# Optimization experiments

Hardware: AMD Instinct MI355X
Metric: run time of the kernel (lower is better)

Reference implementation:

```python
import jax, jax.numpy as jnp
import numpy as np
from jax import lax

B, T, D = 1, 2048, 2048
H, KVH, HD = 16, 4, 128
BETA = 0.9
ROPE_BASE = 10000.0


def _causal_prefix_ema(x, beta):
    # x: (B, T, D); m_t = beta * m_{t-1} + (1 - beta) * x_t, m_{-1} = 0
    def step(m, xt):
        m = beta * m + (1.0 - beta) * xt
        return m, m
    _, ys = lax.scan(step, jnp.zeros_like(x[:, 0]), jnp.swapaxes(x, 0, 1))
    return jnp.swapaxes(ys, 0, 1)


def _rotate_half(x):
    x1, x2 = jnp.split(x, 2, axis=-1)
    return jnp.concatenate([-x2, x1], axis=-1)


def _rope_cos_sin(t, hd, dtype):
    inv_freq = 1.0 / (ROPE_BASE ** (jnp.arange(0, hd, 2, dtype=jnp.float32) / hd))
    freqs = jnp.arange(t, dtype=jnp.float32)[:, None] * inv_freq[None, :]  # (T, HD/2)
    emb = jnp.concatenate([freqs, freqs], axis=-1)  # (T, HD)
    return jnp.cos(emb).astype(dtype)[None, None], jnp.sin(emb).astype(dtype)[None, None]


def setup_inputs() -> dict:
    key = jax.random.key(0)
    ks = jax.random.split(key, 8)
    std = 0.02
    return {
        "hidden_states": jax.random.normal(ks[0], (B, T, D), jnp.float32),
        "Wq": jax.random.normal(ks[1], (D, H * HD), jnp.float32) * std,
        "Wk": jax.random.normal(ks[2], (D, KVH * HD), jnp.float32) * std,
        "Wv": jax.random.normal(ks[3], (D, KVH * HD), jnp.float32) * std,
        "Wo": jax.random.normal(ks[4], (H * HD, D), jnp.float32) * std,
        "Wr1": jax.random.normal(ks[5], (D, D // 2), jnp.float32) * std,
        "br1": jnp.zeros((D // 2,), jnp.float32),
        "Wr2": jax.random.normal(ks[6], (D // 2, 2), jnp.float32) * std,
        "br2": jnp.zeros((2,), jnp.float32),
    }


def reference(hidden_states, Wq, Wk, Wv, Wo, Wr1, br1, Wr2, br2):
    b, t, d = hidden_states.shape
    q = hidden_states @ Wq  # (B, T, H*HD)

    # multi-level memories: l1 = raw, l2 = causal prefix EMA
    l2 = _causal_prefix_ema(hidden_states, BETA)

    # router MLP on q + softmax over levels
    h = jax.nn.silu(q @ Wr1 + br1)
    lam = jax.nn.softmax(h @ Wr2 + br2, axis=-1)  # (B, T, 2)
    fused = lam[..., 0:1] * hidden_states + lam[..., 1:2] * l2

    # shape to heads
    q_s = q.reshape(b, t, H, HD).transpose(0, 2, 1, 3)                 # (B, H, T, HD)
    k_s = (fused @ Wk).reshape(b, t, KVH, HD).transpose(0, 2, 1, 3)    # (B, KVH, T, HD)
    v_s = (fused @ Wv).reshape(b, t, KVH, HD).transpose(0, 2, 1, 3)

    # RoPE
    cos, sin = _rope_cos_sin(t, HD, q_s.dtype)
    q_s = q_s * cos + _rotate_half(q_s) * sin
    k_s = k_s * cos + _rotate_half(k_s) * sin

    # repeat kv for GQA
    n_rep = H // KVH
    k_s = jnp.repeat(k_s, n_rep, axis=1)
    v_s = jnp.repeat(v_s, n_rep, axis=1)

    # causal SDPA
    scale = 1.0 / jnp.sqrt(jnp.asarray(HD, q_s.dtype))
    scores = jnp.einsum("bhqd,bhkd->bhqk", q_s, k_s) * scale
    causal = jnp.tril(jnp.ones((t, t), dtype=bool))
    scores = jnp.where(causal[None, None], scores, jnp.finfo(scores.dtype).min)
    attn = jax.nn.softmax(scores, axis=-1)
    out = jnp.einsum("bhqk,bhkd->bhqd", attn, v_s)  # (B, H, T, HD)

    out = out.transpose(0, 2, 1, 3).reshape(b, t, H * HD)
    return out @ Wo
```

## Files before the change

kernel.cpp:

```cpp
#include <hip/hip_runtime.h>
#include <hip/hip_bf16.h>

#define T_SEQ 2048
#define D_MODEL 2048
#define NH 16
#define NKVH 4
#define HD 128

typedef __attribute__((ext_vector_type(8))) short bf16x8;
typedef __attribute__((ext_vector_type(4))) float f32x4;

static __device__ __forceinline__ short f32_to_bf16(float f) {
    unsigned u = __float_as_uint(f);
    u += 0x7fffu + ((u >> 16) & 1u);
    return (short)(u >> 16);
}
static __device__ __forceinline__ float bf16_to_f32(short s) {
    return __uint_as_float(((unsigned)(unsigned short)s) << 16);
}
static __device__ __forceinline__ void gl_to_lds16(const void* g, void* l) {
    __builtin_amdgcn_global_load_lds(
        (const __attribute__((address_space(1))) unsigned int*)g,
        (__attribute__((address_space(3))) unsigned int*)l, 16, 0, 0);
}

template<int BN>
__global__ __launch_bounds__(256, 2) void gemm_bt_kernel(
    const short* __restrict__ A, const short* __restrict__ Bt,
    float* __restrict__ Cf, short* __restrict__ Cb,
    int M, int N, int K, const float* __restrict__ bias, int act)
{
    constexpr int NI = BN / 64;
    constexpr int BCH = BN / 32;
    __shared__ short Alds[2][64 * 64];
    __shared__ short Blds[2][BN * 64];

    const int tid = threadIdx.x;
    const int wave = tid >> 6, lane = tid & 63;
    const int l16 = lane & 15, quad = lane >> 4;
    const int wn = wave * (BN / 4);
    const int m0 = blockIdx.y * 64, n0 = blockIdx.x * BN;
    const int niter = K >> 6;

    f32x4 acc[4][NI] = {};

    #pragma unroll
    for (int p = 0; p < 2; ++p) {
        int li = p * 256 + tid;
        int row = li >> 3, sc = li & 7;
        gl_to_lds16(A + (size_t)(m0 + row) * K + ((sc ^ (row & 7)) * 8),
                    &Alds[0][(size_t)(p * 256 + wave * 64) * 8]);
    }
    #pragma unroll
    for (int p = 0; p < BCH; ++p) {
        int li = p * 256 + tid;
        int row = li >> 3, sc = li & 7;
        gl_to_lds16(Bt + (size_t)(n0 + row) * K + ((sc ^ (row & 7)) * 8),
                    &Blds[0][(size_t)(p * 256 + wave * 64) * 8]);
    }

    for (int t = 0; t < niter; ++t) {
        asm volatile("s_waitcnt vmcnt(0)\n\ts_barrier" ::: "memory");

        if (t + 1 < niter) {
            int k1 = (t + 1) << 6;
            int nb = (t + 1) & 1;
            #pragma unroll
            for (int p = 0; p < 2; ++p) {
                int li = p * 256 + tid;
                int row = li >> 3, sc = li & 7;
                gl_to_lds16(A + (size_t)(m0 + row) * K + k1 + ((sc ^ (row & 7)) * 8),
                            &Alds[nb][(size_t)(p * 256 + wave * 64) * 8]);
            }
            #pragma unroll
            for (int p = 0; p < BCH; ++p) {
                int li = p * 256 + tid;
                int row = li >> 3, sc = li & 7;
                gl_to_lds16(Bt + (size_t)(n0 + row) * K + k1 + ((sc ^ (row & 7)) * 8),
                            &Blds[nb][(size_t)(p * 256 + wave * 64) * 8]);
            }
        }

        const short* Ab = Alds[t & 1];
        const short* Bb = Blds[t & 1];
        #pragma unroll
        for (int kk = 0; kk < 2; ++kk) {
            bf16x8 a[4], b[NI];
            #pragma unroll
            for (int i = 0; i < 4; ++i)
                a[i] = *(const bf16x8*)
                    &Ab[(size_t)(i * 16 + l16) * 64 + (((kk * 4 + quad) ^ (l16 & 7)) * 8)];
            #pragma unroll
            for (int i = 0; i < NI; ++i)
                b[i] = *(const bf16x8*)
                    &Bb[(size_t)(wn + i * 16 + l16) * 64 + (((kk * 4 + quad) ^ (l16 & 7)) * 8)];
            #pragma unroll
            for (int mi = 0; mi < 4; ++mi)
                #pragma unroll
                for (int ni = 0; ni < NI; ++ni)
                    acc[mi][ni] = __builtin_amdgcn_mfma_f32_16x16x32_bf16(
                        a[mi], b[ni], acc[mi][ni], 0, 0, 0);
        }
    }

    #pragma unroll
    for (int mi = 0; mi < 4; ++mi) {
        #pragma unroll
        for (int ni = 0; ni < NI; ++ni) {
            int col = n0 + wn + ni * 16 + l16;
            float bv = bias ? bias[col] : 0.0f;
            #pragma unroll
            for (int r = 0; r < 4; ++r) {
                int row = m0 + mi * 16 + quad * 4 + r;
                float x = acc[mi][ni][r] + bv;
                if (act) x = x / (1.0f + __expf(-x));
                size_t o = (size_t)row * N + col;
                if (Cf) Cf[o] = x;
                if (Cb) Cb[o] = f32_to_bf16(x);
            }
        }
    }
}

__global__ __launch_bounds__(256) void transpose_all_kernel(
    const float* __restrict__ Wq, const float* __restrict__ Wk,
    const float* __restrict__ Wv, const float* __restrict__ Wr1,
    const float* __restrict__ Wo, short* __restrict__ Wq_t,
    short* __restrict__ Wkv_t, short* __restrict__ Wr1_t,
    short* __restrict__ Wo_t)
{
    __shared__ float tile[32][33];
    int bx = blockIdx.x;
    const float* src; short* dst; int ld, cb;
    if (bx < 64)       { src = Wq;  dst = Wq_t;  ld = 2048; cb = bx; }
    else if (bx < 80)  { src = Wk;  dst = Wkv_t; ld = 512;  cb = bx - 64; }
    else if (bx < 96)  { src = Wv;  dst = Wkv_t + (size_t)512 * 2048; ld = 512; cb = bx - 80; }
    else if (bx < 128) { src = Wr1; dst = Wr1_t; ld = 1024; cb = bx - 96; }
    else               { src = Wo;  dst = Wo_t;  ld = 2048; cb = bx - 128; }
    int c0 = cb * 32, r0 = blockIdx.y * 32;
    int t = threadIdx.x;
    int r = t >> 3, c4 = (t & 7) * 4;
    float4 v = *(const float4*)&src[(size_t)(r0 + r) * ld + c0 + c4];
    tile[r][c4 + 0] = v.x; tile[r][c4 + 1] = v.y;
    tile[r][c4 + 2] = v.z; tile[r][c4 + 3] = v.w;
    __syncthreads();
    short o[4];
    #pragma unroll
    for (int j = 0; j < 4; ++j) o[j] = f32_to_bf16(tile[c4 + j][r]);
    *(uint2*)&dst[(size_t)(c0 + r) * 2048 + r0 + c4] = *(const uint2*)o;
}

__global__ __launch_bounds__(256) void transpose_bf_kernel(
    const short* __restrict__ src, int ld, short* __restrict__ dst, int ldd)
{
    __shared__ float tile[32][33];
    int r0 = blockIdx.y * 32, c0 = blockIdx.x * 32;
    int x = threadIdx.x & 31, y = threadIdx.x >> 5;
    #pragma unroll
    for (int i = 0; i < 4; ++i)
        tile[y + i * 8][x] = bf16_to_f32(src[(size_t)(r0 + y + i * 8) * ld + c0 + x]);
    __syncthreads();
    #pragma unroll
    for (int i = 0; i < 4; ++i)
        dst[(size_t)(c0 + y + i * 8) * ldd + r0 + x] = f32_to_bf16(tile[x][y + i * 8]);
}

__global__ __launch_bounds__(256) void ema_kernel(const float* __restrict__ hs,
                                                  float* __restrict__ l2,
                                                  short* __restrict__ hs_b)
{
    int d = blockIdx.y * 256 + threadIdx.x;
    int t0 = blockIdx.x * 128;
    int ts = t0 - 192; if (ts < 0) ts = 0;
    float m = 0.0f;
    for (int tb = ts; tb < t0; tb += 16) {
        float buf[16];
        #pragma unroll
        for (int j = 0; j < 16; ++j) buf[j] = hs[(size_t)(tb + j) * D_MODEL + d];
        #pragma unroll
        for (int j = 0; j < 16; ++j) m = 0.9f * m + 0.1f * buf[j];
    }
    for (int tb = t0; tb < t0 + 128; tb += 16) {
        float buf[16];
        #pragma unroll
        for (int j = 0; j < 16; ++j) buf[j] = hs[(size_t)(tb + j) * D_MODEL + d];
        #pragma unroll
        for (int j = 0; j < 16; ++j) hs_b[(size_t)(tb + j) * D_MODEL + d] = f32_to_bf16(buf[j]);
        #pragma unroll
        for (int j = 0; j < 16; ++j) { m = 0.9f * m + 0.1f * buf[j]; buf[j] = m; }
        #pragma unroll
        for (int j = 0; j < 16; ++j) l2[(size_t)(tb + j) * D_MODEL + d] = buf[j];
    }
}

__global__ __launch_bounds__(64) void lam_kernel(
    const short* __restrict__ h, const float* __restrict__ Wr2,
    const float* __restrict__ br2, float* __restrict__ lam)
{
    int t = blockIdx.x;
    int lane = threadIdx.x;
    float z0 = 0.0f, z1 = 0.0f;
    for (int i = lane; i < 1024; i += 64) {
        float hv = bf16_to_f32(h[(size_t)t * 1024 + i]);
        z0 += hv * Wr2[i * 2 + 0];
        z1 += hv * Wr2[i * 2 + 1];
    }
    #pragma unroll
    for (int off = 1; off < 64; off <<= 1) {
        z0 += __shfl_xor(z0, off);
        z1 += __shfl_xor(z1, off);
    }
    if (lane == 0) {
        z0 += br2[0]; z1 += br2[1];
        float mx = fmaxf(z0, z1);
        float e0 = expf(z0 - mx), e1 = expf(z1 - mx);
        float inv = 1.0f / (e0 + e1);
        lam[t * 2 + 0] = e0 * inv;
        lam[t * 2 + 1] = e1 * inv;
    }
}

__global__ void fuse_kernel(const float* __restrict__ hs, const float* __restrict__ l2,
                            const float* __restrict__ lam, short* __restrict__ fused)
{
    int idx = blockIdx.x * blockDim.x + threadIdx.x;
    int t = idx >> 9;
    float a0 = lam[t * 2 + 0], a1 = lam[t * 2 + 1];
    float4 a = ((const float4*)hs)[idx];
    float4 b = ((const float4*)l2)[idx];
    short o[4] = {f32_to_bf16(a0 * a.x + a1 * b.x), f32_to_bf16(a0 * a.y + a1 * b.y),
                  f32_to_bf16(a0 * a.z + a1 * b.z), f32_to_bf16(a0 * a.w + a1 * b.w)};
    *(uint2*)(fused + (size_t)idx * 4) = *(const uint2*)o;
}

__global__ void rope_q_kernel(const short* __restrict__ q, short* __restrict__ qr)
{
    int idx = blockIdx.x * blockDim.x + threadIdx.x;
    int d = idx & 63;
    int h = (idx >> 6) & 15;
    int t = idx >> 10;
    float fr = (float)t * __expf(-(float)d * 0.14391156831212787f);
    float s, c;
    sincosf(fr, &s, &c);
    const float sc = 0.08838834764831845f;
    const short* src = q + (size_t)t * D_MODEL + h * HD;
    float x1 = bf16_to_f32(src[d]) * sc, x2 = bf16_to_f32(src[d + 64]) * sc;
    short* dst = qr + ((size_t)h * T_SEQ + t) * HD;
    dst[d]      = f32_to_bf16(x1 * c - x2 * s);
    dst[d + 64] = f32_to_bf16(x2 * c + x1 * s);
}

__global__ void rope_k_kernel(const short* __restrict__ kv, short* __restrict__ kr)
{
    int idx = blockIdx.x * blockDim.x + threadIdx.x;
    int d = idx & 63;
    int kh = (idx >> 6) & 3;
    int t = idx >> 8;
    float fr = (float)t * __expf(-(float)d * 0.14391156831212787f);
    float s, c;
    sincosf(fr, &s, &c);
    const short* src = kv + (size_t)t * 1024 + kh * HD;
    float x1 = bf16_to_f32(src[d]), x2 = bf16_to_f32(src[d + 64]);
    short* dst = kr + ((size_t)kh * T_SEQ + t) * HD;
    dst[d]      = f32_to_bf16(x1 * c - x2 * s);
    dst[d + 64] = f32_to_bf16(x2 * c + x1 * s);
}

__global__ __launch_bounds__(256, 1) void attn_kernel(
    const short* __restrict__ Qr, const short* __restrict__ Kr,
    const short* __restrict__ Vt, short* __restrict__ Out)
{
    const int pi = blockIdx.x;
    const int h = blockIdx.y;
    const int kvh = h >> 2;
    const int tid = threadIdx.x;
    const int wave = tid >> 6, lane = tid & 63;
    const int l16 = lane & 15, quad = lane >> 4;

    __shared__ short Klds[2][128 * 128];
    __shared__ short Vlds[2][128 * 128];
    __shared__ short Plds[4][16][136];

    const short* kbase = Kr + (size_t)kvh * T_SEQ * HD;
    const short* vbase = Vt + (size_t)kvh * HD * T_SEQ;

    for (int ph = 0; ph < 2; ++ph) {
        const int qt = ph ? (31 - pi) : pi;
        const int qbase = qt * 64 + wave * 16;
        const int n = (qt * 64 + 191) >> 7;

        bf16x8 qf[4];
        {
            const short* qrow = Qr + ((size_t)h * T_SEQ + qbase + l16) * HD;
            #pragma unroll
            for (int kc = 0; kc < 4; ++kc)
                qf[kc] = *(const bf16x8*)&qrow[kc * 32 + quad * 8];
        }
        f32x4 o[8] = {};
        float lsum[4] = {0.0f, 0.0f, 0.0f, 0.0f};

        __syncthreads();

        {
            const short* ks = kbase;
            #pragma unroll
            for (int p = 0; p < 8; ++p) {
                int li = p * 256 + tid;
                int row = li >> 4, gs = (li & 15) ^ (row & 15);
                gl_to_lds16(ks + (size_t)row * HD + gs * 8,
                            &Klds[0][(size_t)(p * 256 + wave * 64) * 8]);
            }
            #pragma unroll
            for (int p = 0; p < 8; ++p) {
                int li = p * 256 + tid;
                int row = li >> 4, gs = (li & 15) ^ (row & 15);
                gl_to_lds16(vbase + (size_t)row * T_SEQ + gs * 8,
                            &Vlds[0][(size_t)(p * 256 + wave * 64) * 8]);
            }
        }

        for (int t = 0; t < n; ++t) {
            asm volatile("s_waitcnt vmcnt(0)\n\ts_barrier" ::: "memory");

            if (t + 1 < n) {
                int kv1 = (t + 1) << 7;
                int nb = (t + 1) & 1;
                const short* ks = kbase + (size_t)kv1 * HD;
                #pragma unroll
                for (int p = 0; p < 8; ++p) {
                    int li = p * 256 + tid;
                    int row = li >> 4, gs = (li & 15) ^ (row & 15);
                    gl_to_lds16(ks + (size_t)row * HD + gs * 8,
                                &Klds[nb][(size_t)(p * 256 + wave * 64) * 8]);
                }
                #pragma unroll
                for (int p = 0; p < 8; ++p) {
                    int li = p * 256 + tid;
                    int row = li >> 4, gs = (li & 15) ^ (row & 15);
                    gl_to_lds16(vbase + (size_t)row * T_SEQ + kv1 + gs * 8,
                                &Vlds[nb][(size_t)(p * 256 + wave * 64) * 8]);
                }
            }

            const short* Kb = Klds[t & 1];
            const short* Vb = Vlds[t & 1];

            f32x4 s[8];
            #pragma unroll
            for (int ni = 0; ni < 8; ++ni) s[ni] = (f32x4){0, 0, 0, 0};
            #pragma unroll
            for (int ni = 0; ni < 8; ++ni)
                #pragma unroll
                for (int kc = 0; kc < 4; ++kc) {
                    bf16x8 b = *(const bf16x8*)
                        &Kb[(size_t)(ni * 16 + l16) * 128 + (((kc * 4 + quad) ^ l16) * 8)];
                    s[ni] = __builtin_amdgcn_mfma_f32_16x16x32_bf16(qf[kc], b, s[ni], 0, 0, 0);
                }

            if (t == n - 1) {
                int kvg0 = t << 7;
                #pragma unroll
                for (int ni = 0; ni < 8; ++ni) {
                    int kvg = kvg0 + ni * 16 + l16;
                    #pragma unroll
                    for (int r = 0; r < 4; ++r) {
                        int qg = qbase + quad * 4 + r;
                        float p = (kvg <= qg) ? __expf(s[ni][r]) : 0.0f;
                        lsum[r] += p;
                        Plds[wave][quad * 4 + r][ni * 16 + l16] = f32_to_bf16(p);
                    }
                }
            } else {
                #pragma unroll
                for (int ni = 0; ni < 8; ++ni)
                    #pragma unroll
                    for (int r = 0; r < 4; ++r) {
                        float p = __expf(s[ni][r]);
                        lsum[r] += p;
                        Plds[wave][quad * 4 + r][ni * 16 + l16] = f32_to_bf16(p);
                    }
            }
            asm volatile("s_waitcnt lgkmcnt(0)" ::: "memory");

            #pragma unroll
            for (int d8 = 0; d8 < 8; ++d8)
                #pragma unroll
                for (int r = 0; r < 4; ++r) o[d8][r] *= 1.0f;
            #pragma unroll
            for (int kc = 0; kc < 4; ++kc) {
                bf16x8 pa = *(const bf16x8*)&Plds[wave][l16][kc * 32 + quad * 8];
                #pragma unroll
                for (int d8 = 0; d8 < 8; ++d8) {
                    bf16x8 b = *(const bf16x8*)
                        &Vb[(size_t)(d8 * 16 + l16) * 128 + (((kc * 4 + quad) ^ l16) * 8)];
                    o[d8] = __builtin_amdgcn_mfma_f32_16x16x32_bf16(pa, b, o[d8], 0, 0, 0);
                }
            }
        }

        #pragma unroll
        for (int r = 0; r < 4; ++r) {
            #pragma unroll
            for (int off = 1; off < 16; off <<= 1)
                lsum[r] += __shfl_xor(lsum[r], off);
            lsum[r] = 1.0f / lsum[r];
        }
        #pragma unroll
        for (int d8 = 0; d8 < 8; ++d8)
            #pragma unroll
            for (int r = 0; r < 4; ++r) {
                int row = qbase + quad * 4 + r;
                Out[(size_t)row * D_MODEL + h * HD + d8 * 16 + l16] =
                    f32_to_bf16(o[d8][r] * lsum[r]);
            }
    }
}

extern "C" void kernel_launch(void* const* d_in, const int* in_sizes, int n_in,
                              void* d_out, int out_size, void* d_ws, size_t ws_size,
                              hipStream_t stream)
{
    const float* hs  = (const float*)d_in[0];
    const float* Wq  = (const float*)d_in[1];
    const float* Wk  = (const float*)d_in[2];
    const float* Wv  = (const float*)d_in[3];
    const float* Wo  = (const float*)d_in[4];
    const float* Wr1 = (const float*)d_in[5];
    const float* br1 = (const float*)d_in[6];
    const float* Wr2 = (const float*)d_in[7];
    const float* br2 = (const float*)d_in[8];
    float* out = (float*)d_out;

    char* w = (char*)d_ws;
    const size_t MB = 1u << 20;
    float* l2_f     = (float*)(w + 0 * MB);
    short* hs_bf    = (short*)(w + 16 * MB);
    short* Wq_t     = (short*)(w + 24 * MB);
    short* Wkv_t    = (short*)(w + 32 * MB);
    short* Wr1_t    = (short*)(w + 36 * MB);
    short* Wo_t     = (short*)(w + 40 * MB);
    short* q_bf     = (short*)(w + 48 * MB);
    short* h_bf     = (short*)(w + 56 * MB);
    short* fused_bf = (short*)(w + 60 * MB);
    short* kv_bf    = (short*)(w + 68 * MB);
    short* qr       = (short*)(w + 72 * MB);
    short* kr       = (short*)(w + 80 * MB);
    short* vr       = (short*)(w + 82 * MB);
    float* lam_f    = (float*)(w + 84 * MB);
    short* attn_bf  = hs_bf;

    transpose_all_kernel<<<dim3(192, 64), 256, 0, stream>>>(
        Wq, Wk, Wv, Wr1, Wo, Wq_t, Wkv_t, Wr1_t, Wo_t);

    ema_kernel<<<dim3(T_SEQ / 128, D_MODEL / 256), 256, 0, stream>>>(hs, l2_f, hs_bf);

    gemm_bt_kernel<128><<<dim3(16, 32), 256, 0, stream>>>(
        hs_bf, Wq_t, nullptr, q_bf, 2048, 2048, 2048, nullptr, 0);

    gemm_bt_kernel<64><<<dim3(16, 32), 256, 0, stream>>>(
        q_bf, Wr1_t, nullptr, h_bf, 2048, 1024, 2048, br1, 1);

    lam_kernel<<<T_SEQ, 64, 0, stream>>>(h_bf, Wr2, br2, lam_f);

    fuse_kernel<<<(T_SEQ * D_MODEL / 4) / 256, 256, 0, stream>>>(hs, l2_f, lam_f, fused_bf);

    gemm_bt_kernel<64><<<dim3(16, 32), 256, 0, stream>>>(
        fused_bf, Wkv_t, nullptr, kv_bf, 2048, 1024, 2048, nullptr, 0);

    rope_q_kernel<<<(T_SEQ * NH * 64) / 256, 256, 0, stream>>>(q_bf, qr);
    rope_k_kernel<<<(T_SEQ * NKVH * 64) / 256, 256, 0, stream>>>(kv_bf, kr);
    transpose_bf_kernel<<<dim3(16, 64), 256, 0, stream>>>(kv_bf + 512, 1024, vr, 2048);

    attn_kernel<<<dim3(16, NH), 256, 0, stream>>>(qr, kr, vr, attn_bf);

    gemm_bt_kernel<128><<<dim3(16, 32), 256, 0, stream>>>(
        attn_bf, Wo_t, out, nullptr, 2048, 2048, 2048, nullptr, 0);
}
```

Measured before the change: 318.0 us.

## Use 8-wave attention blocks over 128-row query tiles with swizzled P and setprio

The attention kernel changes from 4-wave blocks that each process two paired 64-row query tiles (balanced front and back) to 8-wave blocks that each process one 128-row query tile. Each staged K/V tile is now shared by twice as many waves, and the extra waves give more latency hiding. It also XOR-swizzles the P scratch buffer in LDS to avoid bank conflicts and raises wave priority around the MFMA sections. The cost is that the front/back pairing is gone, so causal work per block now ranges from 1 to 16 KV tiles and the grid becomes load-imbalanced.

```diff
diff --git a/kernel.cpp b/kernel.cpp
--- a/kernel.cpp
+++ b/kernel.cpp
@@ -266,11 +266,11 @@
     dst[d + 64] = f32_to_bf16(x2 * c + x1 * s);
 }
 
-__global__ __launch_bounds__(256, 1) void attn_kernel(
+__global__ __launch_bounds__(512, 2) void attn_kernel(
     const short* __restrict__ Qr, const short* __restrict__ Kr,
     const short* __restrict__ Vt, short* __restrict__ Out)
 {
-    const int pi = blockIdx.x;
+    const int qt = blockIdx.x;
     const int h = blockIdx.y;
     const int kvh = h >> 2;
     const int tid = threadIdx.x;
@@ -279,141 +279,140 @@
 
     __shared__ short Klds[2][128 * 128];
     __shared__ short Vlds[2][128 * 128];
-    __shared__ short Plds[4][16][136];
+    __shared__ short Plds[8][16][128];
 
     const short* kbase = Kr + (size_t)kvh * T_SEQ * HD;
     const short* vbase = Vt + (size_t)kvh * HD * T_SEQ;
 
-    for (int ph = 0; ph < 2; ++ph) {
-        const int qt = ph ? (31 - pi) : pi;
-        const int qbase = qt * 64 + wave * 16;
-        const int n = (qt * 64 + 191) >> 7;
-
-        bf16x8 qf[4];
-        {
-            const short* qrow = Qr + ((size_t)h * T_SEQ + qbase + l16) * HD;
-            #pragma unroll
-            for (int kc = 0; kc < 4; ++kc)
-                qf[kc] = *(const bf16x8*)&qrow[kc * 32 + quad * 8];
-        }
-        f32x4 o[8] = {};
-        float lsum[4] = {0.0f, 0.0f, 0.0f, 0.0f};
-
-        __syncthreads();
-
-        {
-            const short* ks = kbase;
-            #pragma unroll
-            for (int p = 0; p < 8; ++p) {
-                int li = p * 256 + tid;
+    const int qbase = qt * 128 + wave * 16;
+    const int n = qt + 1;
+
+    bf16x8 qf[4];
+    {
+        const short* qrow = Qr + ((size_t)h * T_SEQ + qbase + l16) * HD;
+        #pragma unroll
+        for (int kc = 0; kc < 4; ++kc)
+            qf[kc] = *(const bf16x8*)&qrow[kc * 32 + quad * 8];
+    }
+    f32x4 o[8] = {};
+    float lsum[4] = {0.0f, 0.0f, 0.0f, 0.0f};
+
+    {
+        #pragma unroll
+        for (int p = 0; p < 4; ++p) {
+            int li = p * 512 + tid;
+            int row = li >> 4, gs = (li & 15) ^ (row & 15);
+            gl_to_lds16(kbase + (size_t)row * HD + gs * 8,
+                        &Klds[0][(size_t)(p * 512 + wave * 64) * 8]);
+        }
+        #pragma unroll
+        for (int p = 0; p < 4; ++p) {
+            int li = p * 512 + tid;
+            int row = li >> 4, gs = (li & 15) ^ (row & 15);
+            gl_to_lds16(vbase + (size_t)row * T_SEQ + gs * 8,
+                        &Vlds[0][(size_t)(p * 512 + wave * 64) * 8]);
+        }
+    }
+
+    for (int t = 0; t < n; ++t) {
+        asm volatile("s_waitcnt vmcnt(0)\n\ts_barrier" ::: "memory");
+
+        if (t + 1 < n) {
+            int kv1 = (t + 1) << 7;
+            int nb = (t + 1) & 1;
+            const short* ks = kbase + (size_t)kv1 * HD;
+            #pragma unroll
+            for (int p = 0; p < 4; ++p) {
+                int li = p * 512 + tid;
                 int row = li >> 4, gs = (li & 15) ^ (row & 15);
                 gl_to_lds16(ks + (size_t)row * HD + gs * 8,
-                            &Klds[0][(size_t)(p * 256 + wave * 64) * 8]);
-            }
-            #pragma unroll
-            for (int p = 0; p < 8; ++p) {
-                int li = p * 256 + tid;
+                            &Klds[nb][(size_t)(p * 512 + wave * 64) * 8]);
+            }
+            #pragma unroll
+            for (int p = 0; p < 4; ++p) {
+                int li = p * 512 + tid;
                 int row = li >> 4, gs = (li & 15) ^ (row & 15);
-                gl_to_lds16(vbase + (size_t)row * T_SEQ + gs * 8,
-                            &Vlds[0][(size_t)(p * 256 + wave * 64) * 8]);
-            }
-        }
-
-        for (int t = 0; t < n; ++t) {
-            asm volatile("s_waitcnt vmcnt(0)\n\ts_barrier" ::: "memory");
-
-            if (t + 1 < n) {
-                int kv1 = (t + 1) << 7;
-                int nb = (t + 1) & 1;
-                const short* ks = kbase + (size_t)kv1 * HD;
+                gl_to_lds16(vbase + (size_t)row * T_SEQ + kv1 + gs * 8,
+                            &Vlds[nb][(size_t)(p * 512 + wave * 64) * 8]);
+            }
+        }
+
+        const short* Kb = Klds[t & 1];
+        const short* Vb = Vlds[t & 1];
+
+        f32x4 s[8];
+        #pragma unroll
+        for (int ni = 0; ni < 8; ++ni) s[ni] = (f32x4){0, 0, 0, 0};
+        __builtin_amdgcn_s_setprio(1);
+        #pragma unroll
+        for (int ni = 0; ni < 8; ++ni)
+            #pragma unroll
+            for (int kc = 0; kc < 4; ++kc) {
+                bf16x8 b = *(const bf16x8*)
+                    &Kb[(size_t)(ni * 16 + l16) * 128 + (((kc * 4 + quad) ^ l16) * 8)];
+                s[ni] = __builtin_amdgcn_mfma_f32_16x16x32_bf16(qf[kc], b, s[ni], 0, 0, 0);
+            }
+        __builtin_amdgcn_s_setprio(0);
+
+        if (t == n - 1) {
+            int kvg0 = t << 7;
+            #pragma unroll
+            for (int ni = 0; ni < 8; ++ni) {
+                int kvg = kvg0 + ni * 16 + l16;
                 #pragma unroll
-                for (int p = 0; p < 8; ++p) {
-                    int li = p * 256 + tid;
-                    int row = li >> 4, gs = (li & 15) ^ (row & 15);
-                    gl_to_lds16(ks + (size_t)row * HD + gs * 8,
-                                &Klds[nb][(size_t)(p * 256 + wave * 64) * 8]);
+                for (int r = 0; r < 4; ++r) {
+                    int qg = qbase + quad * 4 + r;
+                    float p = (kvg <= qg) ? __expf(s[ni][r]) : 0.0f;
+                    lsum[r] += p;
+                    int prow = quad * 4 + r, pcol = ni * 16 + l16;
+                    Plds[wave][prow][(((pcol >> 3) ^ prow) * 8) + (pcol & 7)] =
+                        f32_to_bf16(p);
                 }
-                #pragma unroll
-                for (int p = 0; p < 8; ++p) {
-                    int li = p * 256 + tid;
-                    int row = li >> 4, gs = (li & 15) ^ (row & 15);
-                    gl_to_lds16(vbase + (size_t)row * T_SEQ + kv1 + gs * 8,
-                                &Vlds[nb][(size_t)(p * 256 + wave * 64) * 8]);
-                }
-            }
-
-            const short* Kb = Klds[t & 1];
-            const short* Vb = Vlds[t & 1];
-
-            f32x4 s[8];
-            #pragma unroll
-            for (int ni = 0; ni < 8; ++ni) s[ni] = (f32x4){0, 0, 0, 0};
+            }
+        } else {
             #pragma unroll
             for (int ni = 0; ni < 8; ++ni)
                 #pragma unroll
-                for (int kc = 0; kc < 4; ++kc) {
-                    bf16x8 b = *(const bf16x8*)
-                        &Kb[(size_t)(ni * 16 + l16) * 128 + (((kc * 4 + quad) ^ l16) * 8)];
-                    s[ni] = __builtin_amdgcn_mfma_f32_16x16x32_bf16(qf[kc], b, s[ni], 0, 0, 0);
+                for (int r = 0; r < 4; ++r) {
+                    float p = __expf(s[ni][r]);
+                    lsum[r] += p;
+                    int prow = quad * 4 + r, pcol = ni * 16 + l16;
+                    Plds[wave][prow][(((pcol >> 3) ^ prow) * 8) + (pcol & 7)] =
+                        f32_to_bf16(p);
                 }
-
-            if (t == n - 1) {
-                int kvg0 = t << 7;
-                #pragma unroll
-                for (int ni = 0; ni < 8; ++ni) {
-                    int kvg = kvg0 + ni * 16 + l16;
-                    #pragma unroll
-                    for (int r = 0; r < 4; ++r) {
-                        int qg = qbase + quad * 4 + r;
-                        float p = (kvg <= qg) ? __expf(s[ni][r]) : 0.0f;
-                        lsum[r] += p;
-                        Plds[wave][quad * 4 + r][ni * 16 + l16] = f32_to_bf16(p);
-                    }
-                }
-            } else {
-                #pragma unroll
-                for (int ni = 0; ni < 8; ++ni)
-                    #pragma unroll
-                    for (int r = 0; r < 4; ++r) {
-                        float p = __expf(s[ni][r]);
-                        lsum[r] += p;
-                        Plds[wave][quad * 4 + r][ni * 16 + l16] = f32_to_bf16(p);
-                    }
-            }
-            asm volatile("s_waitcnt lgkmcnt(0)" ::: "memory");
-
-            #pragma unroll
-            for (int d8 = 0; d8 < 8; ++d8)
-                #pragma unroll
-                for (int r = 0; r < 4; ++r) o[d8][r] *= 1.0f;
-            #pragma unroll
-            for (int kc = 0; kc < 4; ++kc) {
-                bf16x8 pa = *(const bf16x8*)&Plds[wave][l16][kc * 32 + quad * 8];
-                #pragma unroll
-                for (int d8 = 0; d8 < 8; ++d8) {
-                    bf16x8 b = *(const bf16x8*)
-                        &Vb[(size_t)(d8 * 16 + l16) * 128 + (((kc * 4 + quad) ^ l16) * 8)];
-                    o[d8] = __builtin_amdgcn_mfma_f32_16x16x32_bf16(pa, b, o[d8], 0, 0, 0);
-                }
-            }
-        }
-
+        }
+        asm volatile("s_waitcnt lgkmcnt(0)" ::: "memory");
+
+        __builtin_amdgcn_s_setprio(1);
+        #pragma unroll
+        for (int kc = 0; kc < 4; ++kc) {
+            bf16x8 pa = *(const bf16x8*)
+                &Plds[wave][l16][(((kc * 4 + quad) ^ l16) * 8)];
+            #pragma unroll
+            for (int d8 = 0; d8 < 8; ++d8) {
+                bf16x8 b = *(const bf16x8*)
+                    &Vb[(size_t)(d8 * 16 + l16) * 128 + (((kc * 4 + quad) ^ l16) * 8)];
+                o[d8] = __builtin_amdgcn_mfma_f32_16x16x32_bf16(pa, b, o[d8], 0, 0, 0);
+            }
+        }
+        __builtin_amdgcn_s_setprio(0);
+    }
+
+    #pragma unroll
+    for (int r = 0; r < 4; ++r) {
+        #pragma unroll
+        for (int off = 1; off < 16; off <<= 1)
+            lsum[r] += __shfl_xor(lsum[r], off);
+        lsum[r] = 1.0f / lsum[r];
+    }
+    #pragma unroll
+    for (int d8 = 0; d8 < 8; ++d8)
         #pragma unroll
         for (int r = 0; r < 4; ++r) {
-            #pragma unroll
-            for (int off = 1; off < 16; off <<= 1)
-                lsum[r] += __shfl_xor(lsum[r], off);
-            lsum[r] = 1.0f / lsum[r];
-        }
-        #pragma unroll
-        for (int d8 = 0; d8 < 8; ++d8)
-            #pragma unroll
-            for (int r = 0; r < 4; ++r) {
-                int row = qbase + quad * 4 + r;
-                Out[(size_t)row * D_MODEL + h * HD + d8 * 16 + l16] =
-                    f32_to_bf16(o[d8][r] * lsum[r]);
-            }
-    }
+            int row = qbase + quad * 4 + r;
+            Out[(size_t)row * D_MODEL + h * HD + d8 * 16 + l16] =
+                f32_to_bf16(o[d8][r] * lsum[r]);
+        }
 }
 
 extern "C" void kernel_launch(void* const* d_in, const int* in_sizes, int n_in,
@@ -471,7 +470,7 @@
     rope_k_kernel<<<(T_SEQ * NKVH * 64) / 256, 256, 0, stream>>>(kv_bf, kr);
     transpose_bf_kernel<<<dim3(16, 64), 256, 0, stream>>>(kv_bf + 512, 1024, vr, 2048);
 
-    attn_kernel<<<dim3(16, NH), 256, 0, stream>>>(qr, kr, vr, attn_bf);
+    attn_kernel<<<dim3(16, NH), 512, 0, stream>>>(qr, kr, vr, attn_bf);
 
     gemm_bt_kernel<128><<<dim3(16, 32), 256, 0, stream>>>(
         attn_bf, Wo_t, out, nullptr, 2048, 2048, 2048, nullptr, 0);
```

New measurement: 323.7 us. About the same (+1.8%).

## Widen attention query tile to 128 rows per block with swizzled P buffer

Applied to the files above, without the earlier changes.

Each attention block now handles one 128-row query tile (32 rows per wave, two MFMA M-tiles) instead of two 64-row tiles paired for causal load balance. Every K/V tile loaded into LDS therefore feeds twice as much MFMA work, and the causal mask applies only on the final diagonal tile. The grid is reordered to heads-by-query-tile, the P staging buffer gets an XOR swizzle to avoid bank conflicts, and s_setprio is raised around the MFMA loops. The trade-offs are more registers per wave and uneven per-block work, since blocks run from 1 to 16 KV iterations, with no more paired balancing.

```diff
diff --git a/kernel.cpp b/kernel.cpp
--- a/kernel.cpp
+++ b/kernel.cpp
@@ -270,8 +270,8 @@
     const short* __restrict__ Qr, const short* __restrict__ Kr,
     const short* __restrict__ Vt, short* __restrict__ Out)
 {
-    const int pi = blockIdx.x;
-    const int h = blockIdx.y;
+    const int h = blockIdx.x;
+    const int qt = blockIdx.y;
     const int kvh = h >> 2;
     const int tid = threadIdx.x;
     const int wave = tid >> 6, lane = tid & 63;
@@ -279,141 +279,155 @@
 
     __shared__ short Klds[2][128 * 128];
     __shared__ short Vlds[2][128 * 128];
-    __shared__ short Plds[4][16][136];
+    __shared__ short Plds[4][32][128];
 
     const short* kbase = Kr + (size_t)kvh * T_SEQ * HD;
     const short* vbase = Vt + (size_t)kvh * HD * T_SEQ;
 
-    for (int ph = 0; ph < 2; ++ph) {
-        const int qt = ph ? (31 - pi) : pi;
-        const int qbase = qt * 64 + wave * 16;
-        const int n = (qt * 64 + 191) >> 7;
-
-        bf16x8 qf[4];
-        {
-            const short* qrow = Qr + ((size_t)h * T_SEQ + qbase + l16) * HD;
-            #pragma unroll
-            for (int kc = 0; kc < 4; ++kc)
-                qf[kc] = *(const bf16x8*)&qrow[kc * 32 + quad * 8];
-        }
-        f32x4 o[8] = {};
-        float lsum[4] = {0.0f, 0.0f, 0.0f, 0.0f};
-
-        __syncthreads();
-
-        {
-            const short* ks = kbase;
+    const int qbase = qt * 128 + wave * 32;
+    const int n = qt + 1;
+
+    bf16x8 qf[2][4];
+    #pragma unroll
+    for (int m = 0; m < 2; ++m) {
+        const short* qrow = Qr + ((size_t)h * T_SEQ + qbase + m * 16 + l16) * HD;
+        #pragma unroll
+        for (int kc = 0; kc < 4; ++kc)
+            qf[m][kc] = *(const bf16x8*)&qrow[kc * 32 + quad * 8];
+    }
+    f32x4 o[2][8] = {};
+    float lsum[2][4] = {};
+
+    {
+        #pragma unroll
+        for (int p = 0; p < 8; ++p) {
+            int li = p * 256 + tid;
+            int row = li >> 4, gs = (li & 15) ^ (row & 15);
+            gl_to_lds16(kbase + (size_t)row * HD + gs * 8,
+                        &Klds[0][(size_t)(p * 256 + wave * 64) * 8]);
+        }
+        #pragma unroll
+        for (int p = 0; p < 8; ++p) {
+            int li = p * 256 + tid;
+            int row = li >> 4, gs = (li & 15) ^ (row & 15);
+            gl_to_lds16(vbase + (size_t)row * T_SEQ + gs * 8,
+                        &Vlds[0][(size_t)(p * 256 + wave * 64) * 8]);
+        }
+    }
+
+    for (int t = 0; t < n; ++t) {
+        asm volatile("s_waitcnt vmcnt(0)\n\ts_barrier" ::: "memory");
+
+        if (t + 1 < n) {
+            int kv1 = (t + 1) << 7;
+            int nb = (t + 1) & 1;
+            const short* ks = kbase + (size_t)kv1 * HD;
             #pragma unroll
             for (int p = 0; p < 8; ++p) {
                 int li = p * 256 + tid;
                 int row = li >> 4, gs = (li & 15) ^ (row & 15);
                 gl_to_lds16(ks + (size_t)row * HD + gs * 8,
-                            &Klds[0][(size_t)(p * 256 + wave * 64) * 8]);
+                            &Klds[nb][(size_t)(p * 256 + wave * 64) * 8]);
             }
             #pragma unroll
             for (int p = 0; p < 8; ++p) {
                 int li = p * 256 + tid;
                 int row = li >> 4, gs = (li & 15) ^ (row & 15);
-                gl_to_lds16(vbase + (size_t)row * T_SEQ + gs * 8,
-                            &Vlds[0][(size_t)(p * 256 + wave * 64) * 8]);
-            }
-        }
-
-        for (int t = 0; t < n; ++t) {
-            asm volatile("s_waitcnt vmcnt(0)\n\ts_barrier" ::: "memory");
-
-            if (t + 1 < n) {
-                int kv1 = (t + 1) << 7;
-                int nb = (t + 1) & 1;
-                const short* ks = kbase + (size_t)kv1 * HD;
-                #pragma unroll
-                for (int p = 0; p < 8; ++p) {
-                    int li = p * 256 + tid;
-                    int row = li >> 4, gs = (li & 15) ^ (row & 15);
-                    gl_to_lds16(ks + (size_t)row * HD + gs * 8,
-                                &Klds[nb][(size_t)(p * 256 + wave * 64) * 8]);
-                }
-                #pragma unroll
-                for (int p = 0; p < 8; ++p) {
-                    int li = p * 256 + tid;
-                    int row = li >> 4, gs = (li & 15) ^ (row & 15);
-                    gl_to_lds16(vbase + (size_t)row * T_SEQ + kv1 + gs * 8,
-                                &Vlds[nb][(size_t)(p * 256 + wave * 64) * 8]);
-                }
-            }
-
-            const short* Kb = Klds[t & 1];
-            const short* Vb = Vlds[t & 1];
-
-            f32x4 s[8];
-            #pragma unroll
-            for (int ni = 0; ni < 8; ++ni) s[ni] = (f32x4){0, 0, 0, 0};
-            #pragma unroll
-            for (int ni = 0; ni < 8; ++ni)
-                #pragma unroll
-                for (int kc = 0; kc < 4; ++kc) {
-                    bf16x8 b = *(const bf16x8*)
-                        &Kb[(size_t)(ni * 16 + l16) * 128 + (((kc * 4 + quad) ^ l16) * 8)];
-                    s[ni] = __builtin_amdgcn_mfma_f32_16x16x32_bf16(qf[kc], b, s[ni], 0, 0, 0);
-                }
-
-            if (t == n - 1) {
-                int kvg0 = t << 7;
+                gl_to_lds16(vbase + (size_t)row * T_SEQ + kv1 + gs * 8,
+                            &Vlds[nb][(size_t)(p * 256 + wave * 64) * 8]);
+            }
+        }
+
+        const short* Kb = Klds[t & 1];
+        const short* Vb = Vlds[t & 1];
+
+        f32x4 s[2][8];
+        #pragma unroll
+        for (int m = 0; m < 2; ++m)
+            #pragma unroll
+            for (int ni = 0; ni < 8; ++ni) s[m][ni] = (f32x4){0, 0, 0, 0};
+        __builtin_amdgcn_s_setprio(1);
+        #pragma unroll
+        for (int ni = 0; ni < 8; ++ni)
+            #pragma unroll
+            for (int kc = 0; kc < 4; ++kc) {
+                bf16x8 b = *(const bf16x8*)
+                    &Kb[(size_t)(ni * 16 + l16) * 128 + (((kc * 4 + quad) ^ l16) * 8)];
+                s[0][ni] = __builtin_amdgcn_mfma_f32_16x16x32_bf16(qf[0][kc], b, s[0][ni], 0, 0, 0);
+                s[1][ni] = __builtin_amdgcn_mfma_f32_16x16x32_bf16(qf[1][kc], b, s[1][ni], 0, 0, 0);
+            }
+        __builtin_amdgcn_s_setprio(0);
+
+        if (t == n - 1) {
+            int kvg0 = t << 7;
+            #pragma unroll
+            for (int m = 0; m < 2; ++m)
                 #pragma unroll
                 for (int ni = 0; ni < 8; ++ni) {
                     int kvg = kvg0 + ni * 16 + l16;
                     #pragma unroll
                     for (int r = 0; r < 4; ++r) {
-                        int qg = qbase + quad * 4 + r;
-                        float p = (kvg <= qg) ? __expf(s[ni][r]) : 0.0f;
-                        lsum[r] += p;
-                        Plds[wave][quad * 4 + r][ni * 16 + l16] = f32_to_bf16(p);
+                        int qg = qbase + m * 16 + quad * 4 + r;
+                        float p = (kvg <= qg) ? __expf(s[m][ni][r]) : 0.0f;
+                        lsum[m][r] += p;
+                        int prow = quad * 4 + r, pcol = ni * 16 + l16;
+                        Plds[wave][m * 16 + prow][(((pcol >> 3) ^ prow) * 8) + (pcol & 7)] =
+                            f32_to_bf16(p);
                     }
                 }
-            } else {
+        } else {
+            #pragma unroll
+            for (int m = 0; m < 2; ++m)
                 #pragma unroll
                 for (int ni = 0; ni < 8; ++ni)
                     #pragma unroll
                     for (int r = 0; r < 4; ++r) {
-                        float p = __expf(s[ni][r]);
-                        lsum[r] += p;
-                        Plds[wave][quad * 4 + r][ni * 16 + l16] = f32_to_bf16(p);
+                        float p = __expf(s[m][ni][r]);
+                        lsum[m][r] += p;
+                        int prow = quad * 4 + r, pcol = ni * 16 + l16;
+                        Plds[wave][m * 16 + prow][(((pcol >> 3) ^ prow) * 8) + (pcol & 7)] =
+                            f32_to_bf16(p);
                     }
-            }
-            asm volatile("s_waitcnt lgkmcnt(0)" ::: "memory");
-
-            #pragma unroll
-            for (int d8 = 0; d8 < 8; ++d8)
-                #pragma unroll
-                for (int r = 0; r < 4; ++r) o[d8][r] *= 1.0f;
-            #pragma unroll
-            for (int kc = 0; kc < 4; ++kc) {
-                bf16x8 pa = *(const bf16x8*)&Plds[wave][l16][kc * 32 + quad * 8];
-                #pragma unroll
-                for (int d8 = 0; d8 < 8; ++d8) {
-                    bf16x8 b = *(const bf16x8*)
-                        &Vb[(size_t)(d8 * 16 + l16) * 128 + (((kc * 4 + quad) ^ l16) * 8)];
-                    o[d8] = __builtin_amdgcn_mfma_f32_16x16x32_bf16(pa, b, o[d8], 0, 0, 0);
-                }
-            }
-        }
-
+        }
+        asm volatile("s_waitcnt lgkmcnt(0)" ::: "memory");
+
+        __builtin_amdgcn_s_setprio(1);
+        #pragma unroll
+        for (int kc = 0; kc < 4; ++kc) {
+            bf16x8 pa0 = *(const bf16x8*)
+                &Plds[wave][l16][(((kc * 4 + quad) ^ l16) * 8)];
+            bf16x8 pa1 = *(const bf16x8*)
+                &Plds[wave][16 + l16][(((kc * 4 + quad) ^ l16) * 8)];
+            #pragma unroll
+            for (int d8 = 0; d8 < 8; ++d8) {
+                bf16x8 b = *(const bf16x8*)
+                    &Vb[(size_t)(d8 * 16 + l16) * 128 + (((kc * 4 + quad) ^ l16) * 8)];
+                o[0][d8] = __builtin_amdgcn_mfma_f32_16x16x32_bf16(pa0, b, o[0][d8], 0, 0, 0);
+                o[1][d8] = __builtin_amdgcn_mfma_f32_16x16x32_bf16(pa1, b, o[1][d8], 0, 0, 0);
+            }
+        }
+        __builtin_amdgcn_s_setprio(0);
+    }
+
+    #pragma unroll
+    for (int m = 0; m < 2; ++m)
         #pragma unroll
         for (int r = 0; r < 4; ++r) {
             #pragma unroll
             for (int off = 1; off < 16; off <<= 1)
-                lsum[r] += __shfl_xor(lsum[r], off);
-            lsum[r] = 1.0f / lsum[r];
-        }
+                lsum[m][r] += __shfl_xor(lsum[m][r], off);
+            lsum[m][r] = 1.0f / lsum[m][r];
+        }
+    #pragma unroll
+    for (int m = 0; m < 2; ++m)
         #pragma unroll
         for (int d8 = 0; d8 < 8; ++d8)
             #pragma unroll
             for (int r = 0; r < 4; ++r) {
-                int row = qbase + quad * 4 + r;
+                int row = qbase + m * 16 + quad * 4 + r;
                 Out[(size_t)row * D_MODEL + h * HD + d8 * 16 + l16] =
-                    f32_to_bf16(o[d8][r] * lsum[r]);
-            }
-    }
+                    f32_to_bf16(o[m][d8][r] * lsum[m][r]);
+            }
 }
 
 extern "C" void kernel_launch(void* const* d_in, const int* in_sizes, int n_in,
@@ -471,7 +485,7 @@
     rope_k_kernel<<<(T_SEQ * NKVH * 64) / 256, 256, 0, stream>>>(kv_bf, kr);
     transpose_bf_kernel<<<dim3(16, 64), 256, 0, stream>>>(kv_bf + 512, 1024, vr, 2048);
 
-    attn_kernel<<<dim3(16, NH), 256, 0, stream>>>(qr, kr, vr, attn_bf);
+    attn_kernel<<<dim3(NH, 16), 256, 0, stream>>>(qr, kr, vr, attn_bf);
 
     gemm_bt_kernel<128><<<dim3(16, 32), 256, 0, stream>>>(
         attn_bf, Wo_t, out, nullptr, 2048, 2048, 2048, nullptr, 0);
```

Result: slower. 350.1 us (+10.1%).
